# Kernel tuning notes

Hardware: AMD Instinct MI355X
Metric: run time of the kernel (lower is better)

Reference implementation:

```python
import jax, jax.numpy as jnp
import numpy as np

D_MODEL = 1024
D_INNER = 2048   # expand * d_model
D_STATE = 16
D_CONV = 4
DT_RANK = 64     # ceil(d_model / 16)
BATCH = 4
SEQ = 4096


def setup_inputs() -> dict:
    key = jax.random.key(0)
    ks = jax.random.split(key, 8)
    nrm = lambda k, shape, scale: jax.random.normal(k, shape, jnp.float32) * scale
    # dt_proj bias init (inverse softplus of dt in [dt_min, dt_max])
    dt_min, dt_max, dt_floor = 1e-3, 1e-1, 1e-4
    dt = jnp.exp(jax.random.uniform(ks[5], (D_INNER,), jnp.float32)
                 * (np.log(dt_max) - np.log(dt_min)) + np.log(dt_min))
    dt = jnp.clip(dt, dt_floor, None)
    b_dt = dt + jnp.log(-jnp.expm1(-dt))
    # A = diag(1..d_state) per channel, stored as log
    A_log = jnp.broadcast_to(jnp.log(jnp.arange(1, D_STATE + 1, dtype=jnp.float32))[None, :],
                             (D_INNER, D_STATE)).copy()
    dt_std = DT_RANK ** -0.5
    return {
        "x": nrm(ks[0], (BATCH, SEQ, D_MODEL), 1.0),
        "W_in": nrm(ks[1], (2 * D_INNER, D_MODEL), 0.02),
        "conv_w": nrm(ks[2], (D_INNER, 1, D_CONV), 0.2),
        "conv_b": jnp.zeros((D_INNER,), jnp.float32),
        "W_x": nrm(ks[3], (DT_RANK + 2 * D_STATE, D_INNER), 0.02),
        "W_dt": jax.random.uniform(ks[4], (D_INNER, DT_RANK), jnp.float32, -dt_std, dt_std),
        "b_dt": b_dt,
        "A_log": A_log,
        "D": jnp.ones((D_INNER,), jnp.float32),
        "W_out": nrm(ks[6], (D_MODEL, D_INNER), 0.02),
    }


def reference(x, W_in, conv_w, conv_b, W_x, W_dt, b_dt, A_log, D, W_out):
    B, T, _ = x.shape
    silu = jax.nn.silu
    # in_proj -> (x_inner, z)
    xz = jnp.einsum('btd,ed->bte', x, W_in)          # (B,T,2*d_inner)
    x_inner, z = jnp.split(xz, 2, axis=-1)
    # causal depthwise conv1d (pad left d_conv-1, equiv to torch pad+slice[:T])
    xp = jnp.pad(x_inner.transpose(0, 2, 1), ((0, 0), (0, 0), (D_CONV - 1, 0)))
    xc = jax.lax.conv_general_dilated(xp, conv_w, (1,), 'VALID',
                                      feature_group_count=D_INNER)  # (B,d_inner,T)
    x_conv = silu(xc + conv_b[None, :, None]).transpose(0, 2, 1)    # (B,T,d_inner)
    # x_proj -> dt_rank | B | C
    x_dbl = jnp.einsum('btd,ed->bte', x_conv, W_x)
    dt_r, B_ssm, C_ssm = jnp.split(x_dbl, [DT_RANK, DT_RANK + D_STATE], axis=-1)
    dt = jax.nn.softplus(jnp.einsum('btr,dr->btd', dt_r, W_dt) + b_dt)  # (B,T,d_inner)
    A = -jnp.exp(A_log)                                                 # (d_inner,d_state)
    # selective scan over time
    def step(s, inp):
        x_t, dt_t, B_t, C_t = inp              # (B,d_inner),(B,d_inner),(B,d_state),(B,d_state)
        dA = jnp.exp(dt_t[:, :, None] * A[None])              # (B,d_inner,d_state)
        s = s * dA + (dt_t * x_t)[:, :, None] * B_t[:, None, :]
        y_t = jnp.einsum('bds,bs->bd', s, C_t)
        return s, y_t

    s0 = jnp.zeros((B, D_INNER, D_STATE), jnp.float32)
    scan_in = (x_conv.transpose(1, 0, 2), dt.transpose(1, 0, 2),
               B_ssm.transpose(1, 0, 2), C_ssm.transpose(1, 0, 2))
    _, ys = jax.lax.scan(step, s0, scan_in)    # (T,B,d_inner)
    y = ys.transpose(1, 0, 2)
    y = y * silu(z) + D * x_conv
    out = jnp.einsum('btd,ed->bte', y, W_out)  # (B,T,d_model)
    return out
```

## Files before the change

### kernel.cpp

```cpp
#include <hip/hip_runtime.h>
#include <hip/hip_bf16.h>
#include <hip/hip_fp16.h>

#define SEQ    4096
#define DMODEL 1024
#define DINNER 2048
#define DSTATE 16
#define DTRANK 64
#define NC     64
#define CL     64
#define SPLITK 4

typedef __bf16 v8bf  __attribute__((ext_vector_type(8)));
typedef float  f32x4 __attribute__((ext_vector_type(4)));
typedef unsigned short u16x8 __attribute__((ext_vector_type(8)));

static __device__ __forceinline__ float bfu2f(unsigned short u) {
    union { float f; unsigned int i; } c; c.i = ((unsigned int)u) << 16; return c.f;
}
static __device__ __forceinline__ unsigned short f2bfu(float f) {
    union { float f; unsigned int i; } c; c.f = f;
    unsigned int r = c.i + 0x7FFFu + ((c.i >> 16) & 1u);
    return (unsigned short)(r >> 16);
}
static __device__ __forceinline__ float h2f(unsigned short u) {
    __half h; *reinterpret_cast<unsigned short*>(&h) = u; return __half2float(h);
}
static __device__ __forceinline__ unsigned short f2h(float f) {
    __half h = __float2half(f); return *reinterpret_cast<unsigned short*>(&h);
}
static __device__ __forceinline__ float softplus_fast(float v) {
    return fmaxf(v, 0.f) + __logf(1.f + __expf(-fabsf(v)));
}

static __device__ __forceinline__ void gload_lds16(const void* g, void* l) {
    __builtin_amdgcn_global_load_lds(
        (const __attribute__((address_space(1))) unsigned int*)g,
        (__attribute__((address_space(3))) unsigned int*)l, 16, 0, 0);
}

static __device__ __forceinline__ void pow16(float e1, float* pw) {
    const float e2 = e1 * e1, e4 = e2 * e2, e8 = e4 * e4;
    pw[0] = e1;        pw[1] = e2;        pw[2] = e2 * e1;   pw[3] = e4;
    pw[4] = e4 * e1;   pw[5] = e4 * e2;   pw[6] = e4 * pw[2]; pw[7] = e8;
    pw[8] = e8 * e1;   pw[9] = e8 * e2;   pw[10] = e8 * pw[2]; pw[11] = e8 * e4;
    pw[12] = e8 * pw[4]; pw[13] = e8 * pw[5]; pw[14] = e8 * pw[6]; pw[15] = e8 * e8;
}

__global__ void detect_kernel(const void* __restrict__ x, int* __restrict__ flag)
{
    const float f = ((const float*)x)[threadIdx.x];
    const float a = fabsf(f);
    const bool ok = (a < 1e20f) && (a > 1e-20f);
    unsigned long long m = __ballot(ok);
    if (threadIdx.x == 0) *flag = (__popcll(m) >= 48) ? 1 : 0;
}

__global__ void prep_kernel(const unsigned short* __restrict__ a_log_b,
                            int* __restrict__ sflag)
{
    __shared__ int ok_sh;
    if (threadIdx.x == 0) ok_sh = 1;
    __syncthreads();
    int ok = 1;
    for (int i = threadIdx.x; i < DINNER * DSTATE; i += 256) {
        const float A = __expf(bfu2f(a_log_b[i]));
        const float n = (float)((i & 15) + 1);
        if (fabsf(A - n) > 0.02f * n) ok = 0;
    }
    if (!ok) atomicAnd(&ok_sh, 0);
    __syncthreads();
    if (threadIdx.x == 0) *sflag = ok_sh;
}

__global__ __launch_bounds__(256) void cvt_kernel(
    const void* __restrict__ src, size_t src_off,
    unsigned short* __restrict__ dst, int n, const int* __restrict__ flagp)
{
    const int f32 = *flagp;
    const int stride = gridDim.x * 256;
    if (f32) {
        const float* s = (const float*)src + src_off;
        for (int i = blockIdx.x * 256 + threadIdx.x; i < n; i += stride)
            dst[i] = f2bfu(s[i]);
    } else {
        const unsigned short* s = (const unsigned short*)src + src_off;
        for (int i = blockIdx.x * 256 + threadIdx.x; i < n; i += stride)
            dst[i] = s[i];
    }
}

__global__ __launch_bounds__(256) void gemm_db(
    const unsigned short* __restrict__ A, int lda,
    const unsigned short* __restrict__ B, int ldb,
    void* __restrict__ Cbase, int row0c, int ldc, int c_ext,
    int N, int K, const int* __restrict__ flagp)
{
    __shared__ __align__(16) unsigned short SM[4 * 128 * 64];

    const int cf32 = c_ext ? *flagp : 0;

    const int tid  = threadIdx.x;
    const int lane = tid & 63;
    const int wave = tid >> 6;
    const int wr   = wave >> 1;
    const int wc   = wave & 1;

    const int nwg = gridDim.x * gridDim.y;
    const int bid = blockIdx.y * gridDim.x + blockIdx.x;
    const int swz = (bid & 7) * (nwg >> 3) + (bid >> 3);
    const int m0  = (swz / gridDim.x) * 128;
    const int n0  = (swz % gridDim.x) * 128;

    f32x4 acc[4][4] = {};

    const int r32 = tid >> 3;
    const int c8  = tid & 7;

    const unsigned short* Arow = A + (size_t)m0 * lda;
    const unsigned short* Brow = B + (size_t)n0 * ldb;

#define STAGE_DB(buf, k0)                                                      \
    {                                                                          \
        _Pragma("unroll")                                                      \
        for (int h = 0; h < 4; ++h) {                                          \
            const int rr = r32 + h * 32;                                       \
            const int lg = (c8 ^ (rr & 7)) * 8;                                \
            gload_lds16(&Arow[(size_t)rr * lda + (k0) + lg],                   \
                        &SM[(buf) * 8192 + rr * 64 + c8 * 8]);                 \
            gload_lds16(&Brow[(size_t)rr * ldb + (k0) + lg],                   \
                        &SM[16384 + (buf) * 8192 + rr * 64 + c8 * 8]);         \
        }                                                                      \
    }

    STAGE_DB(0, 0);
    const int NT = K >> 6;
    int cur = 0;

    for (int kt = 0; kt < NT; ++kt) {
        if (kt + 1 < NT) {
            STAGE_DB(cur ^ 1, (kt + 1) * 64);
            asm volatile("s_waitcnt vmcnt(8)" ::: "memory");
        } else {
            asm volatile("s_waitcnt vmcnt(0)" ::: "memory");
        }
        __builtin_amdgcn_s_barrier();

        const unsigned short* Ab = &SM[cur * 8192];
        const unsigned short* Bb = &SM[16384 + cur * 8192];
        const int lm = lane & 15;
        const int g  = lane >> 4;
#pragma unroll
        for (int ks = 0; ks < 2; ++ks) {
            v8bf a_frag[4], b_frag[4];
#pragma unroll
            for (int i = 0; i < 4; ++i) {
                const int ra = wr * 64 + i * 16 + lm;
                const int rb = wc * 64 + i * 16 + lm;
                a_frag[i] = *reinterpret_cast<const v8bf*>(
                    &Ab[ra * 64 + (((ks * 4 + g) ^ (ra & 7))) * 8]);
                b_frag[i] = *reinterpret_cast<const v8bf*>(
                    &Bb[rb * 64 + (((ks * 4 + g) ^ (rb & 7))) * 8]);
            }
#pragma unroll
            for (int i = 0; i < 4; ++i)
#pragma unroll
                for (int j = 0; j < 4; ++j)
                    acc[i][j] = __builtin_amdgcn_mfma_f32_16x16x32_bf16(
                        a_frag[i], b_frag[j], acc[i][j], 0, 0, 0);
        }
        asm volatile("" ::: "memory");
        __builtin_amdgcn_s_barrier();
        cur ^= 1;
    }
#undef STAGE_DB

    float* eb = reinterpret_cast<float*>(SM);
    {
        const int lm = lane & 15;
        const int lr = (lane >> 4) * 4;
#pragma unroll
        for (int i = 0; i < 4; ++i)
#pragma unroll
            for (int j = 0; j < 4; ++j) {
                const int cl = wc * 64 + j * 16 + lm;
#pragma unroll
                for (int q = 0; q < 4; ++q) {
                    const int row = wr * 64 + i * 16 + lr + q;
                    eb[row * 128 + (cl ^ ((row & 7) << 2))] = acc[i][j][q];
                }
            }
    }
    __syncthreads();
#pragma unroll
    for (int r0 = 0; r0 < 8; ++r0) {
        const int row = (tid >> 4) + r0 * 16;
        const int cb2 = (tid & 15) * 8;
        const int sw  = (row & 7) << 2;
        const f32x4 v0 = *reinterpret_cast<const f32x4*>(&eb[row * 128 + (cb2 ^ sw)]);
        const f32x4 v1 = *reinterpret_cast<const f32x4*>(&eb[row * 128 + ((cb2 + 4) ^ sw)]);
        const size_t gr = (size_t)(row0c + m0 + row) * ldc + n0 + cb2;
        if (cf32) {
            __builtin_nontemporal_store(v0, reinterpret_cast<f32x4*>(&((float*)Cbase)[gr]));
            __builtin_nontemporal_store(v1, reinterpret_cast<f32x4*>(&((float*)Cbase)[gr + 4]));
        } else {
            u16x8 o;
#pragma unroll
            for (int k = 0; k < 4; ++k) { o[k] = f2bfu(v0[k]); o[4 + k] = f2bfu(v1[k]); }
            *reinterpret_cast<u16x8*>(&((unsigned short*)Cbase)[gr]) = o;
        }
    }
}

__global__ __launch_bounds__(256) void gemm_dt(
    const unsigned short* __restrict__ A, int lda,
    const unsigned short* __restrict__ B, int ldb,
    __half* __restrict__ Cbase, int ldc,
    const unsigned short* __restrict__ bias)
{
    __shared__ __align__(16) unsigned short As[128 * 64];
    __shared__ __align__(16) unsigned short Bs[128 * 64];

    const int tid  = threadIdx.x;
    const int lane = tid & 63;
    const int wave = tid >> 6;
    const int wr   = wave >> 1;
    const int wc   = wave & 1;
    const int m0   = blockIdx.y * 128;
    const int n0   = blockIdx.x * 128;

    f32x4 acc[4][4] = {};

    const int r32 = tid >> 3;
    const int c8  = tid & 7;

    {
#pragma unroll
        for (int h = 0; h < 4; ++h) {
            const int rr = r32 + h * 32;
            const int lg = (c8 ^ (rr & 7)) * 8;
            gload_lds16(&A[(size_t)(m0 + rr) * lda + lg], &As[rr * 64 + c8 * 8]);
            gload_lds16(&B[(size_t)(n0 + rr) * ldb + lg], &Bs[rr * 64 + c8 * 8]);
        }
        __syncthreads();

        const int lm = lane & 15;
        const int g  = lane >> 4;
#pragma unroll
        for (int ks = 0; ks < 2; ++ks) {
            v8bf a_frag[4], b_frag[4];
#pragma unroll
            for (int i = 0; i < 4; ++i) {
                const int ra = wr * 64 + i * 16 + lm;
                const int rb = wc * 64 + i * 16 + lm;
                a_frag[i] = *reinterpret_cast<const v8bf*>(
                    &As[ra * 64 + (((ks * 4 + g) ^ (ra & 7))) * 8]);
                b_frag[i] = *reinterpret_cast<const v8bf*>(
                    &Bs[rb * 64 + (((ks * 4 + g) ^ (rb & 7))) * 8]);
            }
#pragma unroll
            for (int i = 0; i < 4; ++i)
#pragma unroll
                for (int j = 0; j < 4; ++j)
                    acc[i][j] = __builtin_amdgcn_mfma_f32_16x16x32_bf16(
                        a_frag[i], b_frag[j], acc[i][j], 0, 0, 0);
        }
    }

    const int lm = lane & 15;
    const int lr = (lane >> 4) * 4;
#pragma unroll
    for (int i = 0; i < 4; ++i) {
#pragma unroll
        for (int j = 0; j < 4; ++j) {
            const int col = n0 + wc * 64 + j * 16 + lm;
            const float bv = bfu2f(bias[col]);
#pragma unroll
            for (int q = 0; q < 4; ++q) {
                const int row = m0 + wr * 64 + i * 16 + lr + q;
                Cbase[(size_t)row * ldc + col] =
                    __float2half(softplus_fast(acc[i][j][q] + bv));
            }
        }
    }
}

__global__ __launch_bounds__(256) void gemm_splitk(
    const unsigned short* __restrict__ A, int lda,
    const unsigned short* __restrict__ B, int ldb,
    float* __restrict__ part, int Mrows,
    int N, int kchunk)
{
    __shared__ __align__(16) unsigned short As[128 * 64];
    __shared__ __align__(16) unsigned short Bs[128 * 64];

    const int tid  = threadIdx.x;
    const int lane = tid & 63;
    const int wave = tid >> 6;
    const int wr   = wave >> 1;
    const int wc   = wave & 1;
    const int m0   = blockIdx.y * 128;
    const int split = blockIdx.z;
    const int kbeg = split * kchunk;

    f32x4 acc[4][4] = {};

    const int r32 = tid >> 3;
    const int c8  = tid & 7;

    for (int k0 = kbeg; k0 < kbeg + kchunk; k0 += 64) {
        __syncthreads();
#pragma unroll
        for (int h = 0; h < 4; ++h) {
            const int rr = r32 + h * 32;
            const int lg = (c8 ^ (rr & 7)) * 8;
            gload_lds16(&A[(size_t)(m0 + rr) * lda + k0 + lg], &As[rr * 64 + c8 * 8]);
            gload_lds16(&B[(size_t)rr * ldb + k0 + lg], &Bs[rr * 64 + c8 * 8]);
        }
        __syncthreads();

        const int lm = lane & 15;
        const int g  = lane >> 4;
#pragma unroll
        for (int ks = 0; ks < 2; ++ks) {
            v8bf a_frag[4], b_frag[4];
#pragma unroll
            for (int i = 0; i < 4; ++i) {
                const int ra = wr * 64 + i * 16 + lm;
                const int rb = wc * 64 + i * 16 + lm;
                a_frag[i] = *reinterpret_cast<const v8bf*>(
                    &As[ra * 64 + (((ks * 4 + g) ^ (ra & 7))) * 8]);
                b_frag[i] = *reinterpret_cast<const v8bf*>(
                    &Bs[rb * 64 + (((ks * 4 + g) ^ (rb & 7))) * 8]);
            }
#pragma unroll
            for (int i = 0; i < 4; ++i)
#pragma unroll
                for (int j = 0; j < 4; ++j)
                    acc[i][j] = __builtin_amdgcn_mfma_f32_16x16x32_bf16(
                        a_frag[i], b_frag[j], acc[i][j], 0, 0, 0);
        }
    }

    const int lm = lane & 15;
    const int lr = (lane >> 4) * 4;
    float* dst = part + (size_t)split * Mrows * 96;
#pragma unroll
    for (int i = 0; i < 4; ++i) {
#pragma unroll
        for (int j = 0; j < 4; ++j) {
            const int col = wc * 64 + j * 16 + lm;
            if (col >= N) continue;
#pragma unroll
            for (int q = 0; q < 4; ++q) {
                const int row = m0 + wr * 64 + i * 16 + lr + q;
                dst[(size_t)row * 96 + col] = acc[i][j][q];
            }
        }
    }
}

__global__ __launch_bounds__(256) void splitk_reduce(
    const float* __restrict__ part, unsigned short* __restrict__ dst,
    float* __restrict__ bcf, int n)
{
    const int i = blockIdx.x * 256 + threadIdx.x;
    if (i >= n) return;
    float s = 0.f;
#pragma unroll
    for (int k = 0; k < SPLITK; ++k) s += part[(size_t)k * n + i];
    dst[i] = f2bfu(s);
    const int m = i / 96;
    const int col = i - m * 96;
    if (col >= 64) bcf[(size_t)m * 32 + (col - 64)] = s;
}

__global__ __launch_bounds__(256) void conv_silu_kernel(
    const unsigned short* __restrict__ xz,
    const unsigned short* __restrict__ cw,
    const unsigned short* __restrict__ cb,
    unsigned short* __restrict__ xc)
{
    const int idx = blockIdx.x * 256 + threadIdx.x;
    const int d2 = idx & 1023;
    const int m = idx >> 10;
    const int t = m & (SEQ - 1);
    const int d = d2 * 2;

    const u16x8 w = *reinterpret_cast<const u16x8*>(&cw[d * 4]);
    const unsigned int bb = *reinterpret_cast<const unsigned int*>(&cb[d]);
    float s0 = bfu2f((unsigned short)(bb & 0xffff));
    float s1 = bfu2f((unsigned short)(bb >> 16));
#pragma unroll
    for (int j = 0; j < 4; ++j) {
        const int tt = t - 3 + j;
        if (tt >= 0) {
            const unsigned int xv = *reinterpret_cast<const unsigned int*>(
                &xz[(size_t)(m - 3 + j) * 4096 + d]);
            s0 += bfu2f(w[j])     * bfu2f((unsigned short)(xv & 0xffff));
            s1 += bfu2f(w[4 + j]) * bfu2f((unsigned short)(xv >> 16));
        }
    }
    const float g0 = s0 / (1.f + __expf(-s0));
    const float g1 = s1 / (1.f + __expf(-s1));
    const unsigned int o = (unsigned int)f2bfu(g0) | ((unsigned int)f2bfu(g1) << 16);
    *reinterpret_cast<unsigned int*>(&xc[(size_t)m * 2048 + d]) = o;
}

__global__ __launch_bounds__(256) void scan_local_kernel(
    const unsigned short* __restrict__ xz,
    const unsigned short* __restrict__ xconv,
    const float* __restrict__ bcf,
    const unsigned short* __restrict__ A_log,
    unsigned short* __restrict__ S,
    float* __restrict__ sumdt,
    const int* __restrict__ sflagp)
{
    const int gid = blockIdx.x * 256 + threadIdx.x;
    const int d = gid & (DINNER - 1);
    const int c = (gid >> 11) & (NC - 1);
    const int b = gid >> 17;
    const int fast = *sflagp;

    float st[16];
#pragma unroll
    for (int s = 0; s < 16; ++s) st[s] = 0.f;
    float sd = 0.f;
    const size_t mb = (size_t)b * SEQ + c * CL;

    float Ar[16];
    if (!fast) {
#pragma unroll
        for (int s = 0; s < 16; ++s) Ar[s] = -__expf(bfu2f(A_log[d * DSTATE + s]));
    }

    for (int t = 0; t < CL; ++t) {
        const size_t m = mb + t;
        const float dt = __half2float(
            reinterpret_cast<const __half*>(xz)[m * 4096 + d]);
        const float x  = bfu2f(xconv[m * DINNER + d]);
        const f32x4 B0 = *reinterpret_cast<const f32x4*>(&bcf[m * 32]);
        const f32x4 B1 = *reinterpret_cast<const f32x4*>(&bcf[m * 32 + 4]);
        const f32x4 B2 = *reinterpret_cast<const f32x4*>(&bcf[m * 32 + 8]);
        const f32x4 B3 = *reinterpret_cast<const f32x4*>(&bcf[m * 32 + 12]);
        const float du = dt * x;
        float pw[16];
        if (fast) {
            pow16(__expf(-dt), pw);
        } else {
#pragma unroll
            for (int s = 0; s < 16; ++s) pw[s] = __expf(dt * Ar[s]);
        }
#pragma unroll
        for (int s = 0; s < 4; ++s) st[s]      = st[s]      * pw[s]      + du * B0[s];
#pragma unroll
        for (int s = 0; s < 4; ++s) st[4 + s]  = st[4 + s]  * pw[4 + s]  + du * B1[s];
#pragma unroll
        for (int s = 0; s < 4; ++s) st[8 + s]  = st[8 + s]  * pw[8 + s]  + du * B2[s];
#pragma unroll
        for (int s = 0; s < 4; ++s) st[12 + s] = st[12 + s] * pw[12 + s] + du * B3[s];
        sd += dt;
    }
    const size_t o = (((size_t)b * NC + c) * DINNER + d) * DSTATE;
    u16x8 h0, h1;
#pragma unroll
    for (int s = 0; s < 8; ++s) { h0[s] = f2h(st[s]); h1[s] = f2h(st[8 + s]); }
    *reinterpret_cast<u16x8*>(&S[o]) = h0;
    *reinterpret_cast<u16x8*>(&S[o + 8]) = h1;
    sumdt[((size_t)b * NC + c) * DINNER + d] = sd;
}

__global__ __launch_bounds__(256) void scan_carry_kernel(
    const unsigned short* __restrict__ A_log,
    unsigned short* __restrict__ S,
    const float* __restrict__ sumdt)
{
    const int gid = blockIdx.x * 256 + threadIdx.x;
    const int s = gid & 15;
    const int d = (gid >> 4) & (DINNER - 1);
    const int b = gid >> 15;

    const float A = -__expf(bfu2f(A_log[d * DSTATE + s]));
    float carry = 0.f;
    for (int c = 0; c < NC; ++c) {
        const size_t o = (((size_t)b * NC + c) * DINNER + d) * DSTATE + s;
        const float se = h2f(S[o]);
        S[o] = f2h(carry);
        carry = carry * __expf(A * sumdt[((size_t)b * NC + c) * DINNER + d]) + se;
    }
}

__global__ __launch_bounds__(256) void scan_final_kernel(
    unsigned short* __restrict__ xz,
    const unsigned short* __restrict__ xconv,
    const float* __restrict__ bcf,
    const unsigned short* __restrict__ A_log,
    const unsigned short* __restrict__ Dvec,
    const unsigned short* __restrict__ S,
    const int* __restrict__ sflagp)
{
    const int gid = blockIdx.x * 256 + threadIdx.x;
    const int d = gid & (DINNER - 1);
    const int c = (gid >> 11) & (NC - 1);
    const int b = gid >> 17;
    const int fast = *sflagp;

    const float Dv = bfu2f(Dvec[d]);
    float st[16];
    const size_t o = (((size_t)b * NC + c) * DINNER + d) * DSTATE;
    {
        const u16x8 h0 = *reinterpret_cast<const u16x8*>(&S[o]);
        const u16x8 h1 = *reinterpret_cast<const u16x8*>(&S[o + 8]);
#pragma unroll
        for (int s = 0; s < 8; ++s) { st[s] = h2f(h0[s]); st[8 + s] = h2f(h1[s]); }
    }
    const size_t mb = (size_t)b * SEQ + c * CL;

    float Ar[16];
    if (!fast) {
#pragma unroll
        for (int s = 0; s < 16; ++s) Ar[s] = -__expf(bfu2f(A_log[d * DSTATE + s]));
    }

    for (int t = 0; t < CL; ++t) {
        const size_t m = mb + t;
        const float dt = __half2float(
            reinterpret_cast<const __half*>(xz)[m * 4096 + d]);
        const float x  = bfu2f(xconv[m * DINNER + d]);
        const f32x4 B0 = *reinterpret_cast<const f32x4*>(&bcf[m * 32]);
        const f32x4 B1 = *reinterpret_cast<const f32x4*>(&bcf[m * 32 + 4]);
        const f32x4 B2 = *reinterpret_cast<const f32x4*>(&bcf[m * 32 + 8]);
        const f32x4 B3 = *reinterpret_cast<const f32x4*>(&bcf[m * 32 + 12]);
        const f32x4 C0 = *reinterpret_cast<const f32x4*>(&bcf[m * 32 + 16]);
        const f32x4 C1 = *reinterpret_cast<const f32x4*>(&bcf[m * 32 + 20]);
        const f32x4 C2 = *reinterpret_cast<const f32x4*>(&bcf[m * 32 + 24]);
        const f32x4 C3 = *reinterpret_cast<const f32x4*>(&bcf[m * 32 + 28]);
        const float du = dt * x;
        float pw[16];
        if (fast) {
            pow16(__expf(-dt), pw);
        } else {
#pragma unroll
            for (int s = 0; s < 16; ++s) pw[s] = __expf(dt * Ar[s]);
        }
        float p0 = 0.f, p1 = 0.f, p2 = 0.f, p3 = 0.f;
#pragma unroll
        for (int s = 0; s < 4; ++s) {
            st[s] = st[s] * pw[s] + du * B0[s];           p0 += st[s] * C0[s];
        }
#pragma unroll
        for (int s = 0; s < 4; ++s) {
            st[4 + s] = st[4 + s] * pw[4 + s] + du * B1[s];   p1 += st[4 + s] * C1[s];
        }
#pragma unroll
        for (int s = 0; s < 4; ++s) {
            st[8 + s] = st[8 + s] * pw[8 + s] + du * B2[s];   p2 += st[8 + s] * C2[s];
        }
#pragma unroll
        for (int s = 0; s < 4; ++s) {
            st[12 + s] = st[12 + s] * pw[12 + s] + du * B3[s]; p3 += st[12 + s] * C3[s];
        }
        const float p = (p0 + p1) + (p2 + p3);
        const float z = bfu2f(xz[m * 4096 + DINNER + d]);
        const float sig = 1.f / (1.f + __expf(-z));
        xz[m * 4096 + d] = f2bfu(p * (z * sig) + Dv * x);
    }
}

extern "C" void kernel_launch(void* const* d_in, const int* in_sizes, int n_in,
                              void* d_out, int out_size, void* d_ws, size_t ws_size,
                              hipStream_t stream)
{
    const void* x     = d_in[0];
    const void* W_in  = d_in[1];
    const void* convw = d_in[2];
    const void* convb = d_in[3];
    const void* W_x   = d_in[4];
    const void* W_dt  = d_in[5];
    const void* b_dt  = d_in[6];
    const void* A_log = d_in[7];
    const void* Dv    = d_in[8];
    const void* W_out = d_in[9];

    char* ws = (char*)d_ws;
    size_t off = 256;
    int* flag  = (int*)ws;
    int* sflag = (int*)ws + 16;
    auto arena = [&](size_t bytes) {
        char* p = ws + off;
        off += (bytes + 255) & ~(size_t)255;
        return p;
    };
    unsigned short* w_in_b  = (unsigned short*)arena((size_t)4096 * 1024 * 2);
    unsigned short* convw_b = (unsigned short*)arena(8192 * 2);
    unsigned short* convb_b = (unsigned short*)arena(2048 * 2);
    unsigned short* w_x_b   = (unsigned short*)arena((size_t)96 * 2048 * 2);
    unsigned short* w_dt_b  = (unsigned short*)arena((size_t)2048 * 64 * 2);
    unsigned short* b_dt_b  = (unsigned short*)arena(2048 * 2);
    unsigned short* a_log_b = (unsigned short*)arena((size_t)2048 * 16 * 2);
    unsigned short* dv_b    = (unsigned short*)arena(2048 * 2);
    unsigned short* w_out_b = (unsigned short*)arena((size_t)1024 * 2048 * 2);
    const size_t fixed = off;

    const size_t U_per_b  = (size_t)SEQ * 1024 * 2;
    const size_t per_batch =
        (size_t)SEQ * 4096 * 2 + (size_t)SEQ * 2048 * 2 + (size_t)SEQ * 96 * 2 +
        U_per_b;
    int CB = 4;
    while (CB > 1 && fixed + (size_t)CB * per_batch > ws_size) CB >>= 1;
    const int nchunks = 4 / CB;
    const int Mc = CB * SEQ;

    unsigned short* xz    = (unsigned short*)(ws + fixed);
    unsigned short* xconv = xz + (size_t)Mc * 4096;
    unsigned short* xdbl  = xconv + (size_t)Mc * 2048;
    char*           U     = (char*)(xdbl + (size_t)Mc * 96);
    unsigned short* x_bf  = (unsigned short*)U;
    float*          xpart = (float*)U;
    float*          bcf   = (float*)(U + (size_t)SPLITK * Mc * 96 * 4);
    unsigned short* S     = (unsigned short*)U;
    float*          sumdt = (float*)(U + (size_t)CB * NC * 2048 * DSTATE * 2);

    detect_kernel<<<1, 64, 0, stream>>>(x, flag);

    cvt_kernel<<<1024, 256, 0, stream>>>(W_in,  0, w_in_b,  4096 * 1024, flag);
    cvt_kernel<<<32,   256, 0, stream>>>(convw, 0, convw_b, 8192,        flag);
    cvt_kernel<<<8,    256, 0, stream>>>(convb, 0, convb_b, 2048,        flag);
    cvt_kernel<<<256,  256, 0, stream>>>(W_x,   0, w_x_b,   96 * 2048,   flag);
    cvt_kernel<<<256,  256, 0, stream>>>(W_dt,  0, w_dt_b,  2048 * 64,   flag);
    cvt_kernel<<<8,    256, 0, stream>>>(b_dt,  0, b_dt_b,  2048,        flag);
    cvt_kernel<<<64,   256, 0, stream>>>(A_log, 0, a_log_b, 2048 * 16,   flag);
    cvt_kernel<<<8,    256, 0, stream>>>(Dv,    0, dv_b,    2048,        flag);
    cvt_kernel<<<1024, 256, 0, stream>>>(W_out, 0, w_out_b, 1024 * 2048, flag);
    prep_kernel<<<1, 256, 0, stream>>>(a_log_b, sflag);

    for (int cchunk = 0; cchunk < nchunks; ++cchunk) {
        const int row0 = cchunk * Mc;

        cvt_kernel<<<4096, 256, 0, stream>>>(
            x, (size_t)row0 * DMODEL, x_bf, Mc * DMODEL, flag);

        gemm_db<<<dim3(4096 / 128, Mc / 128), 256, 0, stream>>>(
            x_bf, DMODEL, w_in_b, DMODEL, xz, 0, 4096, 0, 4096, DMODEL, flag);

        conv_silu_kernel<<<(Mc * DINNER) / 512, 256, 0, stream>>>(
            xz, convw_b, convb_b, xconv);

        gemm_splitk<<<dim3(1, Mc / 128, SPLITK), 256, 0, stream>>>(
            xconv, DINNER, w_x_b, DINNER, xpart, Mc, 96, DINNER / SPLITK);
        splitk_reduce<<<(Mc * 96 + 255) / 256, 256, 0, stream>>>(
            xpart, xdbl, bcf, Mc * 96);

        gemm_dt<<<dim3(DINNER / 128, Mc / 128), 256, 0, stream>>>(
            xdbl, 96, w_dt_b, DTRANK, (__half*)xz, 4096, b_dt_b);

        scan_local_kernel<<<(CB * NC * DINNER) / 256, 256, 0, stream>>>(
            xz, xconv, bcf, a_log_b, S, sumdt, sflag);
        scan_carry_kernel<<<(CB * DINNER * DSTATE) / 256, 256, 0, stream>>>(
            a_log_b, S, sumdt);
        scan_final_kernel<<<(CB * NC * DINNER) / 256, 256, 0, stream>>>(
            xz, xconv, bcf, a_log_b, dv_b, S, sflag);

        gemm_db<<<dim3(DMODEL / 128, Mc / 128), 256, 0, stream>>>(
            xz, 4096, w_out_b, DINNER, d_out, row0, DMODEL, 1,
            DMODEL, DINNER, flag);
    }
}
```

Measured before the change: 696.6 us.

## Batch weight conversions, double-buffer split-K GEMM, stage dt GEMM output via LDS

Nine separate weight-conversion launches are merged into one batched kernel that uses a 2D grid indexed by tensor. The split-K x_proj GEMM gets double-buffered LDS tiles with explicit vmcnt waits, so global loads overlap MFMA work. The dt GEMM epilogue now writes fp16 results to a swizzled LDS tile and then emits 16-byte coalesced global stores instead of scattered 2-byte writes. The cost is more LDS per block, which may lower occupancy, plus hand-written waitcnt logic that must match the number of outstanding loads.

```diff
diff --git a/kernel.cpp b/kernel.cpp
--- a/kernel.cpp
+++ b/kernel.cpp
@@ -85,6 +85,30 @@
             dst[i] = f2bfu(s[i]);
     } else {
         const unsigned short* s = (const unsigned short*)src + src_off;
+        for (int i = blockIdx.x * 256 + threadIdx.x; i < n; i += stride)
+            dst[i] = s[i];
+    }
+}
+
+struct CvtBatch {
+    const void* src[9];
+    unsigned short* dst[9];
+    int n[9];
+};
+__global__ __launch_bounds__(256) void cvt9_kernel(CvtBatch jb,
+                                                   const int* __restrict__ flagp)
+{
+    const int f32 = *flagp;
+    const int t = blockIdx.y;
+    const int n = jb.n[t];
+    unsigned short* __restrict__ dst = jb.dst[t];
+    const int stride = gridDim.x * 256;
+    if (f32) {
+        const float* __restrict__ s = (const float*)jb.src[t];
+        for (int i = blockIdx.x * 256 + threadIdx.x; i < n; i += stride)
+            dst[i] = f2bfu(s[i]);
+    } else {
+        const unsigned short* __restrict__ s = (const unsigned short*)jb.src[t];
         for (int i = blockIdx.x * 256 + threadIdx.x; i < n; i += stride)
             dst[i] = s[i];
     }
@@ -215,11 +239,10 @@
 __global__ __launch_bounds__(256) void gemm_dt(
     const unsigned short* __restrict__ A, int lda,
     const unsigned short* __restrict__ B, int ldb,
-    __half* __restrict__ Cbase, int ldc,
+    unsigned short* __restrict__ Cbase, int ldc,
     const unsigned short* __restrict__ bias)
 {
-    __shared__ __align__(16) unsigned short As[128 * 64];
-    __shared__ __align__(16) unsigned short Bs[128 * 64];
+    __shared__ __align__(16) unsigned short SM[2 * 128 * 64];
 
     const int tid  = threadIdx.x;
     const int lane = tid & 63;
@@ -234,6 +257,8 @@
     const int r32 = tid >> 3;
     const int c8  = tid & 7;
 
+    unsigned short* As = SM;
+    unsigned short* Bs = SM + 8192;
     {
 #pragma unroll
         for (int h = 0; h < 4; ++h) {
@@ -267,21 +292,35 @@
         }
     }
 
-    const int lm = lane & 15;
-    const int lr = (lane >> 4) * 4;
-#pragma unroll
-    for (int i = 0; i < 4; ++i) {
-#pragma unroll
-        for (int j = 0; j < 4; ++j) {
-            const int col = n0 + wc * 64 + j * 16 + lm;
-            const float bv = bfu2f(bias[col]);
-#pragma unroll
-            for (int q = 0; q < 4; ++q) {
-                const int row = m0 + wr * 64 + i * 16 + lr + q;
-                Cbase[(size_t)row * ldc + col] =
-                    __float2half(softplus_fast(acc[i][j][q] + bv));
+    __syncthreads();
+    unsigned short* eb16 = SM;
+    {
+        const int lm = lane & 15;
+        const int lr = (lane >> 4) * 4;
+#pragma unroll
+        for (int i = 0; i < 4; ++i)
+#pragma unroll
+            for (int j = 0; j < 4; ++j) {
+                const int cl = wc * 64 + j * 16 + lm;
+                const float bv = bfu2f(bias[n0 + cl]);
+#pragma unroll
+                for (int q = 0; q < 4; ++q) {
+                    const int row = wr * 64 + i * 16 + lr + q;
+                    const int pos = row * 128 +
+                        ((((cl >> 3) ^ (row & 7)) << 3) | (cl & 7));
+                    eb16[pos] = f2h(softplus_fast(acc[i][j][q] + bv));
+                }
             }
-        }
+    }
+    __syncthreads();
+#pragma unroll
+    for (int r0 = 0; r0 < 8; ++r0) {
+        const int row = (tid >> 4) + r0 * 16;
+        const int ch  = tid & 15;
+        const u16x8 v = *reinterpret_cast<const u16x8*>(
+            &eb16[row * 128 + ((ch ^ (row & 7)) << 3)]);
+        *reinterpret_cast<u16x8*>(
+            &Cbase[(size_t)(m0 + row) * ldc + n0 + ch * 8]) = v;
     }
 }
 
@@ -291,8 +330,7 @@
     float* __restrict__ part, int Mrows,
     int N, int kchunk)
 {
-    __shared__ __align__(16) unsigned short As[128 * 64];
-    __shared__ __align__(16) unsigned short Bs[128 * 64];
+    __shared__ __align__(16) unsigned short SM[4 * 128 * 64];
 
     const int tid  = threadIdx.x;
     const int lane = tid & 63;
@@ -308,17 +346,34 @@
     const int r32 = tid >> 3;
     const int c8  = tid & 7;
 
-    for (int k0 = kbeg; k0 < kbeg + kchunk; k0 += 64) {
-        __syncthreads();
-#pragma unroll
-        for (int h = 0; h < 4; ++h) {
-            const int rr = r32 + h * 32;
-            const int lg = (c8 ^ (rr & 7)) * 8;
-            gload_lds16(&A[(size_t)(m0 + rr) * lda + k0 + lg], &As[rr * 64 + c8 * 8]);
-            gload_lds16(&B[(size_t)rr * ldb + k0 + lg], &Bs[rr * 64 + c8 * 8]);
-        }
-        __syncthreads();
-
+#define STAGE_SK(buf, k0)                                                      \
+    {                                                                          \
+        _Pragma("unroll")                                                      \
+        for (int h = 0; h < 4; ++h) {                                          \
+            const int rr = r32 + h * 32;                                       \
+            const int lg = (c8 ^ (rr & 7)) * 8;                                \
+            gload_lds16(&A[(size_t)(m0 + rr) * lda + (k0) + lg],               \
+                        &SM[(buf) * 8192 + rr * 64 + c8 * 8]);                 \
+            gload_lds16(&B[(size_t)rr * ldb + (k0) + lg],                      \
+                        &SM[16384 + (buf) * 8192 + rr * 64 + c8 * 8]);         \
+        }                                                                      \
+    }
+
+    STAGE_SK(0, kbeg);
+    const int NT = kchunk >> 6;
+    int cur = 0;
+
+    for (int kt = 0; kt < NT; ++kt) {
+        if (kt + 1 < NT) {
+            STAGE_SK(cur ^ 1, kbeg + (kt + 1) * 64);
+            asm volatile("s_waitcnt vmcnt(8)" ::: "memory");
+        } else {
+            asm volatile("s_waitcnt vmcnt(0)" ::: "memory");
+        }
+        __builtin_amdgcn_s_barrier();
+
+        const unsigned short* Ab = &SM[cur * 8192];
+        const unsigned short* Bb = &SM[16384 + cur * 8192];
         const int lm = lane & 15;
         const int g  = lane >> 4;
 #pragma unroll
@@ -329,9 +384,9 @@
                 const int ra = wr * 64 + i * 16 + lm;
                 const int rb = wc * 64 + i * 16 + lm;
                 a_frag[i] = *reinterpret_cast<const v8bf*>(
-                    &As[ra * 64 + (((ks * 4 + g) ^ (ra & 7))) * 8]);
+                    &Ab[ra * 64 + (((ks * 4 + g) ^ (ra & 7))) * 8]);
                 b_frag[i] = *reinterpret_cast<const v8bf*>(
-                    &Bs[rb * 64 + (((ks * 4 + g) ^ (rb & 7))) * 8]);
+                    &Bb[rb * 64 + (((ks * 4 + g) ^ (rb & 7))) * 8]);
             }
 #pragma unroll
             for (int i = 0; i < 4; ++i)
@@ -340,7 +395,11 @@
                     acc[i][j] = __builtin_amdgcn_mfma_f32_16x16x32_bf16(
                         a_frag[i], b_frag[j], acc[i][j], 0, 0, 0);
         }
-    }
+        asm volatile("" ::: "memory");
+        __builtin_amdgcn_s_barrier();
+        cur ^= 1;
+    }
+#undef STAGE_SK
 
     const int lm = lane & 15;
     const int lr = (lane >> 4) * 4;
@@ -436,8 +495,7 @@
 
     for (int t = 0; t < CL; ++t) {
         const size_t m = mb + t;
-        const float dt = __half2float(
-            reinterpret_cast<const __half*>(xz)[m * 4096 + d]);
+        const float dt = h2f(xz[m * 4096 + d]);
         const float x  = bfu2f(xconv[m * DINNER + d]);
         const f32x4 B0 = *reinterpret_cast<const f32x4*>(&bcf[m * 32]);
         const f32x4 B1 = *reinterpret_cast<const f32x4*>(&bcf[m * 32 + 4]);
@@ -524,8 +582,7 @@
 
     for (int t = 0; t < CL; ++t) {
         const size_t m = mb + t;
-        const float dt = __half2float(
-            reinterpret_cast<const __half*>(xz)[m * 4096 + d]);
+        const float dt = h2f(xz[m * 4096 + d]);
         const float x  = bfu2f(xconv[m * DINNER + d]);
         const f32x4 B0 = *reinterpret_cast<const f32x4*>(&bcf[m * 32]);
         const f32x4 B1 = *reinterpret_cast<const f32x4*>(&bcf[m * 32 + 4]);
@@ -623,15 +680,17 @@
 
     detect_kernel<<<1, 64, 0, stream>>>(x, flag);
 
-    cvt_kernel<<<1024, 256, 0, stream>>>(W_in,  0, w_in_b,  4096 * 1024, flag);
-    cvt_kernel<<<32,   256, 0, stream>>>(convw, 0, convw_b, 8192,        flag);
-    cvt_kernel<<<8,    256, 0, stream>>>(convb, 0, convb_b, 2048,        flag);
-    cvt_kernel<<<256,  256, 0, stream>>>(W_x,   0, w_x_b,   96 * 2048,   flag);
-    cvt_kernel<<<256,  256, 0, stream>>>(W_dt,  0, w_dt_b,  2048 * 64,   flag);
-    cvt_kernel<<<8,    256, 0, stream>>>(b_dt,  0, b_dt_b,  2048,        flag);
-    cvt_kernel<<<64,   256, 0, stream>>>(A_log, 0, a_log_b, 2048 * 16,   flag);
-    cvt_kernel<<<8,    256, 0, stream>>>(Dv,    0, dv_b,    2048,        flag);
-    cvt_kernel<<<1024, 256, 0, stream>>>(W_out, 0, w_out_b, 1024 * 2048, flag);
+    CvtBatch jb;
+    jb.src[0] = W_in;  jb.dst[0] = w_in_b;  jb.n[0] = 4096 * 1024;
+    jb.src[1] = convw; jb.dst[1] = convw_b; jb.n[1] = 8192;
+    jb.src[2] = convb; jb.dst[2] = convb_b; jb.n[2] = 2048;
+    jb.src[3] = W_x;   jb.dst[3] = w_x_b;   jb.n[3] = 96 * 2048;
+    jb.src[4] = W_dt;  jb.dst[4] = w_dt_b;  jb.n[4] = 2048 * 64;
+    jb.src[5] = b_dt;  jb.dst[5] = b_dt_b;  jb.n[5] = 2048;
+    jb.src[6] = A_log; jb.dst[6] = a_log_b; jb.n[6] = 2048 * 16;
+    jb.src[7] = Dv;    jb.dst[7] = dv_b;    jb.n[7] = 2048;
+    jb.src[8] = W_out; jb.dst[8] = w_out_b; jb.n[8] = 1024 * 2048;
+    cvt9_kernel<<<dim3(256, 9), 256, 0, stream>>>(jb, flag);
     prep_kernel<<<1, 256, 0, stream>>>(a_log_b, sflag);
 
     for (int cchunk = 0; cchunk < nchunks; ++cchunk) {
@@ -652,7 +711,7 @@
             xpart, xdbl, bcf, Mc * 96);
 
         gemm_dt<<<dim3(DINNER / 128, Mc / 128), 256, 0, stream>>>(
-            xdbl, 96, w_dt_b, DTRANK, (__half*)xz, 4096, b_dt_b);
+            xdbl, 96, w_dt_b, DTRANK, xz, 4096, b_dt_b);
 
         scan_local_kernel<<<(CB * NC * DINNER) / 256, 256, 0, stream>>>(
             xz, xconv, bcf, a_log_b, S, sumdt, sflag);
```

New measurement: 685.8 us. No clear change (-1.6%).
